# Performance work log

Measured on AMD Instinct MI355X. Metric: run time of the kernel, lower is better.

## Reference

```python
import jax, jax.numpy as jnp
import numpy as np

N_IN = 28
N_MID = 256
N_OUT = 28
SEQ = 28
BATCH = 4096


def setup_inputs() -> dict:
    key = jax.random.key(0)
    ks = jax.random.split(key, 8)
    s_ih = 1.0 / np.sqrt(N_MID)
    x = jax.random.normal(ks[0], (BATCH, SEQ, N_IN), dtype=jnp.float32)
    # PyTorch nn.GRU params: weight_ih_l0 [3H, in], weight_hh_l0 [3H, H], biases [3H]
    w_ih = jax.random.uniform(ks[1], (3 * N_MID, N_IN), minval=-s_ih, maxval=s_ih, dtype=jnp.float32)
    w_hh = jax.random.uniform(ks[2], (3 * N_MID, N_MID), minval=-s_ih, maxval=s_ih, dtype=jnp.float32)
    b_ih = jax.random.uniform(ks[3], (3 * N_MID,), minval=-s_ih, maxval=s_ih, dtype=jnp.float32)
    b_hh = jax.random.uniform(ks[4], (3 * N_MID,), minval=-s_ih, maxval=s_ih, dtype=jnp.float32)
    fc_w = jax.random.uniform(ks[5], (N_OUT, N_MID), minval=-s_ih, maxval=s_ih, dtype=jnp.float32)
    fc_b = jax.random.uniform(ks[6], (N_OUT,), minval=-s_ih, maxval=s_ih, dtype=jnp.float32)
    return {"x": x, "w_ih": w_ih, "w_hh": w_hh, "b_ih": b_ih, "b_hh": b_hh,
            "fc_w": fc_w, "fc_b": fc_b}


def _gru_last_hidden(x, w_ih, w_hh, b_ih, b_hh):
    B, T, _ = x.shape
    H = w_hh.shape[1]
    # Precompute input projection for all timesteps: [B, T, 3H]
    gi_all = jnp.einsum('bti,gi->btg', x, w_ih) + b_ih
    gi_all = jnp.moveaxis(gi_all, 1, 0)  # [T, B, 3H]

    def step(h, gi):
        gh = h @ w_hh.T + b_hh  # [B, 3H]
        i_r, i_z, i_n = jnp.split(gi, 3, axis=-1)
        h_r, h_z, h_n = jnp.split(gh, 3, axis=-1)
        r = jax.nn.sigmoid(i_r + h_r)
        z = jax.nn.sigmoid(i_z + h_z)
        n = jnp.tanh(i_n + r * h_n)
        h_new = (1.0 - z) * n + z * h
        return h_new, None

    h0 = jnp.zeros((B, H), dtype=x.dtype)
    h_last, _ = jax.lax.scan(step, h0, gi_all)
    return h_last


def reference(x, w_ih, w_hh, b_ih, b_hh, fc_w, fc_b):
    h_last = _gru_last_hidden(x, w_ih, w_hh, b_ih, b_hh)
    return h_last @ fc_w.T + fc_b
```

## Files before the change

kernel.cpp:

```cpp
#include <hip/hip_runtime.h>
#include <hip/hip_bf16.h>
#include <math.h>

#define N_IN 28
#define N_MID 256
#define N_OUT 28
#define SEQ 28
#define BATCH 4096
#define G3 768
#define ROWS 16
#define THREADS 512
#define NBLK (BATCH / ROWS)

typedef __attribute__((ext_vector_type(8))) short bf16x8;
typedef __attribute__((ext_vector_type(4))) float f32x4;

#define MFMA(a, b, c) __builtin_amdgcn_mfma_f32_16x16x32_bf16((a), (b), (c), 0, 0, 0)

__device__ __forceinline__ f32x4 splat4(float v) {
    f32x4 r;
    r[0] = v; r[1] = v; r[2] = v; r[3] = v;
    return r;
}

__device__ __forceinline__ short f2bf(float v) {
    __hip_bfloat16 b = __float2bfloat16(v);
    return *reinterpret_cast<short*>(&b);
}
__device__ __forceinline__ float bf2f(short s) {
    unsigned int u = ((unsigned int)(unsigned short)s) << 16;
    return __uint_as_float(u);
}
__device__ __forceinline__ unsigned cvt_pk_bf16(float a, float b) {
    unsigned d;
    asm("v_cvt_pk_bf16_f32 %0, %1, %2" : "=v"(d) : "v"(a), "v"(b));
    return d;
}
__device__ __forceinline__ float frcp(float v) {
    return __builtin_amdgcn_rcpf(v);
}
__device__ __forceinline__ float fsigmoid(float v) {
    return frcp(1.0f + __expf(-v));
}
__device__ __forceinline__ float ftanh(float v) {
    float e = __expf(2.0f * v);
    return fmaf(-2.0f, frcp(e + 1.0f), 1.0f);
}

__global__ void prep_w(const float* __restrict__ w_hh, const float* __restrict__ w_ih,
                       const float* __restrict__ b_ih, const float* __restrict__ b_hh,
                       short* __restrict__ wB, short* __restrict__ wI) {
    int idx = blockIdx.x * 256 + threadIdx.x;
    if (idx < G3 * N_MID) wB[idx] = f2bf(w_hh[idx]);
    if (idx < G3 * 32) {
        int g = idx >> 5, k = idx & 31;
        float v = 0.0f;
        if (k < N_IN) {
            v = w_ih[g * N_IN + k];
        } else if (k == 28 || k == 29) {
            float bias = (g < 2 * N_MID) ? (b_ih[g] + b_hh[g]) : b_ih[g];
            v = (k == 28) ? bias : (bias - bf2f(f2bf(bias)));
        }
        wI[idx] = f2bf(v);
    }
}

template<bool HID, int RB, bool LAST>
__device__ __forceinline__ void gru_step(
    int t, const float* __restrict__ x, int rowbase,
    int l15, int lg, int wv, int lane,
    short (&hl)[2][32][17][8],
    const short (&wlds)[2][3][16][64][8],
    const bf16x8 (&wreg)[3][2][6],
    const bf16x8 (&wireg)[3][2],
    const float (&bHN)[2],
    float (&hold)[2][4], const int (&colA)[2],
    float4 &xA, float4 &xB)
{
    constexpr int WB = RB ^ 1;

    float4 nA, nB;
    if (!LAST) {
        const float* xp =
            x + (size_t)(rowbase + l15) * (SEQ * N_IN) + (t + 1) * N_IN + lg * 8;
        nA = *(const float4*)xp;
        nB.x = 0.f; nB.y = 0.f; nB.z = 0.f; nB.w = 0.f;
        if (lg < 3) nB = *(const float4*)(xp + 4);
    }

    const f32x4 zero4 = splat4(0.0f);
    f32x4 aR[2], aZ[2], aIN[2], aHN[2];

    if constexpr (HID) {
        constexpr int ord[8] = {6, 7, 0, 1, 2, 3, 4, 5};
        bf16x8 ah2[2];
        ah2[0] = *(const bf16x8*)&hl[RB][ord[0] * 4 + lg][l15][0];
        __builtin_amdgcn_s_setprio(1);
        #pragma unroll
        for (int i = 0; i < 8; ++i) {
            const int ks = ord[i];
            const int cur = i & 1, nxt = cur ^ 1;
            if (i < 7)
                ah2[nxt] = *(const bf16x8*)&hl[RB][ord[i + 1] * 4 + lg][l15][0];
            #pragma unroll
            for (int a = 0; a < 2; ++a) {
                bf16x8 b0, b1, b2;
                if (ks < 6) {
                    b0 = wreg[0][a][ks]; b1 = wreg[1][a][ks]; b2 = wreg[2][a][ks];
                } else {
                    const int cg = 2 * wv + a;
                    b0 = *(const bf16x8*)&wlds[ks - 6][0][cg][lane][0];
                    b1 = *(const bf16x8*)&wlds[ks - 6][1][cg][lane][0];
                    b2 = *(const bf16x8*)&wlds[ks - 6][2][cg][lane][0];
                }
                if (i == 0) {
                    f32x4 cHN = splat4(bHN[a]);
                    aR[a]  = MFMA(ah2[cur], b0, zero4);
                    aZ[a]  = MFMA(ah2[cur], b1, zero4);
                    aHN[a] = MFMA(ah2[cur], b2, cHN);
                } else {
                    aR[a]  = MFMA(ah2[cur], b0, aR[a]);
                    aZ[a]  = MFMA(ah2[cur], b1, aZ[a]);
                    aHN[a] = MFMA(ah2[cur], b2, aHN[a]);
                }
            }
        }
        __builtin_amdgcn_s_setprio(0);
    }

    float xv[8] = {xA.x, xA.y, xA.z, xA.w, xB.x, xB.y, xB.z, xB.w};
    bf16x8 xh, xlo;
    #pragma unroll
    for (int e = 0; e < 8; ++e) {
        unsigned int u = __float_as_uint(xv[e]);
        xh[e] = (short)(u >> 16);
        float rem = xv[e] - __uint_as_float(u & 0xffff0000u);
        xlo[e] = (short)(__float_as_uint(rem) >> 16);
    }
    if (lg == 3) {
        xh[4] = (short)0x3F80;
        xh[5] = (short)0x3F80;
    }
    #pragma unroll
    for (int a = 0; a < 2; ++a) {
        if constexpr (HID) {
            aR[a]  = MFMA(xh, wireg[0][a], aR[a]);
            aZ[a]  = MFMA(xh, wireg[1][a], aZ[a]);
            aIN[a] = MFMA(xh, wireg[2][a], zero4);
        } else {
            aR[a]  = MFMA(xh, wireg[0][a], zero4);
            aZ[a]  = MFMA(xh, wireg[1][a], zero4);
            aIN[a] = MFMA(xh, wireg[2][a], zero4);
            aHN[a] = splat4(bHN[a]);
        }
        aIN[a] = MFMA(xlo, wireg[2][a], aIN[a]);
    }

    #pragma unroll
    for (int a = 0; a < 2; ++a) {
        const int c = colA[a];
        float hn4[4];
        #pragma unroll
        for (int j = 0; j < 4; ++j) {
            float r = fsigmoid(aR[a][j]);
            float z = fsigmoid(aZ[a][j]);
            float n = ftanh(aIN[a][j] + r * aHN[a][j]);
            float hnew = fmaf(z, hold[a][j] - n, n);
            hold[a][j] = hnew;
            hn4[j] = hnew;
        }
        unsigned p01 = cvt_pk_bf16(hn4[0], hn4[1]);
        unsigned p23 = cvt_pk_bf16(hn4[2], hn4[3]);
        short* bp = &hl[WB][c >> 3][4 * lg][c & 7];
        bp[0]  = (short)(p01 & 0xffffu);
        bp[8]  = (short)(p01 >> 16);
        bp[16] = (short)(p23 & 0xffffu);
        bp[24] = (short)(p23 >> 16);
    }

    if (!LAST) { xA = nA; xB = nB; }
    __syncthreads();
}

__global__ __launch_bounds__(THREADS, 2) void gru_onecu(
    const float* __restrict__ x,
    const short* __restrict__ wB,
    const short* __restrict__ wI,
    const float* __restrict__ b_hh,
    const float* __restrict__ fc_w,
    const float* __restrict__ fc_b,
    float* __restrict__ out)
{
    __shared__ short wlds[2][3][16][64][8];
    __shared__ short hl[2][32][17][8];

    const int tid  = threadIdx.x;
    const int lane = tid & 63;
    const int l15  = lane & 15;
    const int lg   = lane >> 4;
    const int wv   = tid >> 6;
    const int rowbase = blockIdx.x * ROWS;

    for (int idx = tid; idx < 2 * 3 * 16 * 64; idx += THREADS) {
        int L    = idx & 63;
        int frag = idx >> 6;
        int ksl  = frag / 48;
        int rem  = frag - ksl * 48;
        int g    = rem >> 4;
        int cg   = rem & 15;
        int col  = cg * 16 + (L & 15);
        int k0   = (6 + ksl) * 32 + (L >> 4) * 8;
        *(bf16x8*)&wlds[ksl][g][cg][L][0] =
            *(const bf16x8*)(wB + ((size_t)(g * 256 + col)) * 256 + k0);
    }

    bf16x8 wreg[3][2][6];
    bf16x8 wireg[3][2];
    int   colA[2];
    float bHN[2];
    #pragma unroll
    for (int a = 0; a < 2; ++a) {
        const int c = wv * 32 + a * 16 + l15;
        colA[a] = c;
        bHN[a]  = b_hh[512 + c];
        #pragma unroll
        for (int g = 0; g < 3; ++g) {
            wireg[g][a] = *(const bf16x8*)(wI + ((size_t)(g * 256 + c)) * 32 + lg * 8);
            #pragma unroll
            for (int ks = 0; ks < 6; ++ks)
                wreg[g][a][ks] =
                    *(const bf16x8*)(wB + ((size_t)(g * 256 + c)) * 256 + ks * 32 + lg * 8);
        }
    }

    float hold[2][4] = {};

    float4 xA, xB;
    {
        const float* xp = x + (size_t)(rowbase + l15) * (SEQ * N_IN) + lg * 8;
        xA = *(const float4*)xp;
        xB.x = 0.f; xB.y = 0.f; xB.z = 0.f; xB.w = 0.f;
        if (lg < 3) xB = *(const float4*)(xp + 4);
    }

    __syncthreads();

    gru_step<false, 0, false>(0, x, rowbase, l15, lg, wv, lane, hl, wlds, wreg,
                              wireg, bHN, hold, colA, xA, xB);
    for (int tt = 1; tt < SEQ - 1; tt += 2) {
        gru_step<true, 1, false>(tt, x, rowbase, l15, lg, wv, lane, hl, wlds, wreg,
                                 wireg, bHN, hold, colA, xA, xB);
        gru_step<true, 0, false>(tt + 1, x, rowbase, l15, lg, wv, lane, hl, wlds, wreg,
                                 wireg, bHN, hold, colA, xA, xB);
    }
    gru_step<true, 1, true>(SEQ - 1, x, rowbase, l15, lg, wv, lane, hl, wlds, wreg,
                            wireg, bHN, hold, colA, xA, xB);

    float* hf = (float*)&wlds[0][0][0][0][0];
    {
        int r = tid >> 5, kg = tid & 31;
        #pragma unroll
        for (int e = 0; e < 8; ++e) {
            int k = kg * 8 + e;
            hf[r * 256 + k] = bf2f(hl[0][k >> 3][r][k & 7]);
        }
    }
    __syncthreads();
    if (tid < ROWS * N_OUT) {
        int r = tid / N_OUT, o = tid - r * N_OUT;
        float acc = fc_b[o];
        #pragma unroll
        for (int k4 = 0; k4 < 64; ++k4) {
            float4 hv = *(const float4*)&hf[r * 256 + k4 * 4];
            float4 wv4 = *(const float4*)&fc_w[o * 256 + k4 * 4];
            acc = fmaf(hv.x, wv4.x, acc);
            acc = fmaf(hv.y, wv4.y, acc);
            acc = fmaf(hv.z, wv4.z, acc);
            acc = fmaf(hv.w, wv4.w, acc);
        }
        out[(size_t)(rowbase + r) * N_OUT + o] = acc;
    }
}

extern "C" void kernel_launch(void* const* d_in, const int* in_sizes, int n_in,
                              void* d_out, int out_size, void* d_ws, size_t ws_size,
                              hipStream_t stream) {
    const float* x    = (const float*)d_in[0];
    const float* w_ih = (const float*)d_in[1];
    const float* w_hh = (const float*)d_in[2];
    const float* b_ih = (const float*)d_in[3];
    const float* b_hh = (const float*)d_in[4];
    const float* fc_w = (const float*)d_in[5];
    const float* fc_b = (const float*)d_in[6];
    float* out = (float*)d_out;

    short* wB = (short*)d_ws;
    short* wI = wB + G3 * N_MID;

    hipLaunchKernelGGL(prep_w, dim3(768), dim3(256), 0, stream,
                       w_hh, w_ih, b_ih, b_hh, wB, wI);
    hipLaunchKernelGGL(gru_onecu, dim3(NBLK), dim3(THREADS), 0, stream,
                       x, wB, wI, b_hh, fc_w, fc_b, out);
}
```

Measured before the change: 83.55 us.

## Fold log2e scaling into GRU weights and drop x low-part MFMA

Pre-scales the recurrent and input weights and biases by log2(e) (or 2*log2(e) for the candidate gate) in the prep kernel, so the activations can use exp2 directly without a multiply. It also converts x to bf16 with packed round-to-nearest instead of an explicit hi/lo split, and drops the extra MFMA on the low part for the n gate. This trims VALU work and one MFMA per column group on the serial per-step path. The cost is lower input precision for the n-gate projection, plus some extra rounding from scaling the weights before the bf16 conversion.

New measurement: 77.16 us. 7.6% less time.

```diff
diff --git a/kernel.cpp b/kernel.cpp
--- a/kernel.cpp
+++ b/kernel.cpp
@@ -12,6 +12,9 @@
 #define THREADS 512
 #define NBLK (BATCH / ROWS)
 
+#define LOG2E  1.44269504f
+#define LOG2E2 2.88539008f
+
 typedef __attribute__((ext_vector_type(8))) short bf16x8;
 typedef __attribute__((ext_vector_type(4))) float f32x4;
 
@@ -39,26 +42,37 @@
 __device__ __forceinline__ float frcp(float v) {
     return __builtin_amdgcn_rcpf(v);
 }
-__device__ __forceinline__ float fsigmoid(float v) {
-    return frcp(1.0f + __expf(-v));
-}
-__device__ __forceinline__ float ftanh(float v) {
-    float e = __expf(2.0f * v);
-    return fmaf(-2.0f, frcp(e + 1.0f), 1.0f);
+__device__ __forceinline__ float fexp2(float v) {
+#if __has_builtin(__builtin_amdgcn_exp2f)
+    return __builtin_amdgcn_exp2f(v);
+#else
+    return __expf(v * 0.69314718f);
+#endif
+}
+__device__ __forceinline__ float fsigmoid2(float v) {
+    return frcp(1.0f + fexp2(-v));
+}
+__device__ __forceinline__ float ftanh2(float v) {
+    return fmaf(-2.0f, frcp(1.0f + fexp2(v)), 1.0f);
 }
 
 __global__ void prep_w(const float* __restrict__ w_hh, const float* __restrict__ w_ih,
                        const float* __restrict__ b_ih, const float* __restrict__ b_hh,
                        short* __restrict__ wB, short* __restrict__ wI) {
     int idx = blockIdx.x * 256 + threadIdx.x;
-    if (idx < G3 * N_MID) wB[idx] = f2bf(w_hh[idx]);
+    if (idx < G3 * N_MID) {
+        int g = idx >> 8;
+        float s = (g < 2 * N_MID) ? LOG2E : LOG2E2;
+        wB[idx] = f2bf(w_hh[idx] * s);
+    }
     if (idx < G3 * 32) {
         int g = idx >> 5, k = idx & 31;
+        float s = (g < 2 * N_MID) ? LOG2E : LOG2E2;
         float v = 0.0f;
         if (k < N_IN) {
-            v = w_ih[g * N_IN + k];
+            v = w_ih[g * N_IN + k] * s;
         } else if (k == 28 || k == 29) {
-            float bias = (g < 2 * N_MID) ? (b_ih[g] + b_hh[g]) : b_ih[g];
+            float bias = ((g < 2 * N_MID) ? (b_ih[g] + b_hh[g]) : b_ih[g]) * s;
             v = (k == 28) ? bias : (bias - bf2f(f2bf(bias)));
         }
         wI[idx] = f2bf(v);
@@ -129,17 +143,15 @@
     }
 
     float xv[8] = {xA.x, xA.y, xA.z, xA.w, xB.x, xB.y, xB.z, xB.w};
-    bf16x8 xh, xlo;
-    #pragma unroll
-    for (int e = 0; e < 8; ++e) {
-        unsigned int u = __float_as_uint(xv[e]);
-        xh[e] = (short)(u >> 16);
-        float rem = xv[e] - __uint_as_float(u & 0xffff0000u);
-        xlo[e] = (short)(__float_as_uint(rem) >> 16);
-    }
-    if (lg == 3) {
-        xh[4] = (short)0x3F80;
-        xh[5] = (short)0x3F80;
+    unsigned w0 = cvt_pk_bf16(xv[0], xv[1]);
+    unsigned w1 = cvt_pk_bf16(xv[2], xv[3]);
+    unsigned w2 = cvt_pk_bf16(xv[4], xv[5]);
+    unsigned w3 = cvt_pk_bf16(xv[6], xv[7]);
+    if (lg == 3) w2 = 0x3F803F80u;
+    bf16x8 xh;
+    {
+        unsigned* xu = (unsigned*)&xh;
+        xu[0] = w0; xu[1] = w1; xu[2] = w2; xu[3] = w3;
     }
     #pragma unroll
     for (int a = 0; a < 2; ++a) {
@@ -153,7 +165,6 @@
             aIN[a] = MFMA(xh, wireg[2][a], zero4);
             aHN[a] = splat4(bHN[a]);
         }
-        aIN[a] = MFMA(xlo, wireg[2][a], aIN[a]);
     }
 
     #pragma unroll
@@ -162,9 +173,9 @@
         float hn4[4];
         #pragma unroll
         for (int j = 0; j < 4; ++j) {
-            float r = fsigmoid(aR[a][j]);
-            float z = fsigmoid(aZ[a][j]);
-            float n = ftanh(aIN[a][j] + r * aHN[a][j]);
+            float r = fsigmoid2(aR[a][j]);
+            float z = fsigmoid2(aZ[a][j]);
+            float n = ftanh2(aIN[a][j] + r * aHN[a][j]);
             float hnew = fmaf(z, hold[a][j] - n, n);
             hold[a][j] = hnew;
             hn4[j] = hnew;
@@ -222,7 +233,7 @@
     for (int a = 0; a < 2; ++a) {
         const int c = wv * 32 + a * 16 + l15;
         colA[a] = c;
-        bHN[a]  = b_hh[512 + c];
+        bHN[a]  = b_hh[512 + c] * LOG2E2;
         #pragma unroll
         for (int g = 0; g < 3; ++g) {
             wireg[g][a] = *(const bf16x8*)(wI + ((size_t)(g * 256 + c)) * 32 + lg * 8);
```
